# Kernel optimization log

Hardware: AMD Instinct MI355X
Metric: run time of the kernel (lower is better)

Reference implementation:

```python
import jax, jax.numpy as jnp
import numpy as np

D = 256
H = 8

def setup_inputs() -> dict:
    key = jax.random.key(0)
    ks = jax.random.split(key, 6)
    b, n = 4, 2048
    X = jax.random.normal(ks[0], (b, n, D), dtype=jnp.float32)
    s = 1.0 / np.sqrt(D)
    Wq = jax.random.normal(ks[1], (D, D * H), dtype=jnp.float32) * s
    Wk = jax.random.normal(ks[2], (D, D * H), dtype=jnp.float32) * s
    Wv = jax.random.normal(ks[3], (D, D * H), dtype=jnp.float32) * s
    Wo = jax.random.normal(ks[4], (D * H, D), dtype=jnp.float32) * (1.0 / np.sqrt(D * H))
    bo = jnp.zeros((D,), dtype=jnp.float32)
    return {"X": X, "Wq": Wq, "Wk": Wk, "Wv": Wv, "Wo": Wo, "bo": bo}

def reference(X, Wq, Wk, Wv, Wo, bo):
    b, n, _ = X.shape
    scale = D ** (-0.25)
    # project and split heads: [b, n, H, D]
    q = (X @ Wq).reshape(b, n, H, D) * scale
    k = (X @ Wk).reshape(b, n, H, D) * scale
    v = (X @ Wv).reshape(b, n, H, D)
    # attention scores [b, H, n, n]
    scores = jnp.einsum("bqhd,bkhd->bhqk", q, k)
    attn = jax.nn.softmax(scores, axis=-1)
    out = jnp.einsum("bhqk,bkhd->bqhd", attn, v).reshape(b, n, H * D)
    return out @ Wo + bo
```

## Files before the change

### kernel.cpp

```cpp
#include <hip/hip_runtime.h>
#include <hip/hip_bf16.h>
#include <stdint.h>


using short8 = __attribute__((ext_vector_type(8))) short;
using f32x4  = __attribute__((ext_vector_type(4))) float;
using f32x16 = __attribute__((ext_vector_type(16))) float;

#define MFMA16(a, b, c) __builtin_amdgcn_mfma_f32_16x16x32_bf16((a), (b), (c), 0, 0, 0)
#define MFMA32(a, b, c) __builtin_amdgcn_mfma_f32_32x32x16_bf16((a), (b), (c), 0, 0, 0)

#if __has_builtin(__builtin_amdgcn_exp2f)
#define EXP2(x) __builtin_amdgcn_exp2f(x)
#else
#define EXP2(x) exp2f(x)
#endif

__device__ __forceinline__ uint16_t f2bf(float f) {
  union { float f; uint32_t u; } v; v.f = f;
  uint32_t u = v.u;
  u += 0x7fffu + ((u >> 16) & 1u);
  return (uint16_t)(u >> 16);
}

__device__ __forceinline__ uint32_t cvtpk_bf16(float lo, float hi) {
  uint32_t r;
  asm("v_cvt_pk_bf16_f32 %0, %1, %2" : "=v"(r) : "v"(lo), "v"(hi));
  return r;
}

__device__ __forceinline__ void swap32(uint32_t& a, uint32_t& b) {
  asm volatile("v_permlane32_swap_b32 %0, %1" : "+v"(a), "+v"(b));
}

__device__ __forceinline__ void gll16(const void* g, void* l) {
  __builtin_amdgcn_global_load_lds(
      (const __attribute__((address_space(1))) void*)g,
      (__attribute__((address_space(3))) void*)l, 16, 0, 0);
}

__global__ __launch_bounds__(256) void cast_x_k(const float* __restrict__ X,
                                                uint16_t* __restrict__ Xb, int n4) {
  int i = blockIdx.x * 256 + threadIdx.x;
  if (i >= n4) return;
  float4 v = ((const float4*)X)[i];
  union { uint16_t u[4]; uint2 p; } r;
  r.u[0] = f2bf(v.x); r.u[1] = f2bf(v.y); r.u[2] = f2bf(v.z); r.u[3] = f2bf(v.w);
  ((uint2*)Xb)[i] = r.p;
}

__global__ __launch_bounds__(256) void tcast_k(const float* __restrict__ W,
                                               uint16_t* __restrict__ Wt,
                                               int R, int C, float scale) {
  __shared__ float T[64][65];
  int c0 = blockIdx.x * 64, r0 = blockIdx.y * 64;
  int tid = threadIdx.x;
  int cc = tid & 63;
  for (int rr = tid >> 6; rr < 64; rr += 4)
    T[rr][cc] = W[(size_t)(r0 + rr) * C + c0 + cc];
  __syncthreads();
  int n = tid >> 2, kb = (tid & 3) * 16;
  uint16_t* orow = Wt + (size_t)(c0 + n) * R + r0 + kb;
#pragma unroll
  for (int j = 0; j < 16; ++j) orow[j] = f2bf(T[kb + j][n] * scale);
}

template <int EPI>
__global__ __launch_bounds__(256) void gemm_bt_k(const uint16_t* __restrict__ A,
                                                 const uint16_t* __restrict__ Bt,
                                                 void* __restrict__ Cv,
                                                 const float* __restrict__ bias,
                                                 int M, int N, int K) {
  __shared__ uint16_t As[128 * 64];
  __shared__ uint16_t Bs[128 * 64];
  const int tid = threadIdx.x;
  const int wv = tid >> 6, lane = tid & 63;
  const int ql = lane & 15, gq = lane >> 4;
  const int wr = wv >> 1, wc = wv & 1;
  const int m0 = blockIdx.y * 128, n0 = blockIdx.x * 128;

  f32x4 acc[4][4];
#pragma unroll
  for (int i = 0; i < 4; ++i)
#pragma unroll
    for (int j = 0; j < 4; ++j) acc[i][j] = (f32x4){0.f, 0.f, 0.f, 0.f};

  const int nkb = K >> 6;
  for (int kb = 0; kb < nkb; ++kb) {
#pragma unroll
    for (int j = 0; j < 4; ++j) {
      int s = (wv * 4 + j) * 64 + lane;
      int row = s >> 3, c = s & 7;
      int gc = c ^ (row & 7);
      gll16(A + (size_t)(m0 + row) * K + kb * 64 + gc * 8, &As[(wv * 4 + j) * 512]);
      gll16(Bt + (size_t)(n0 + row) * K + kb * 64 + gc * 8, &Bs[(wv * 4 + j) * 512]);
    }
    __syncthreads();

    short8 af[4][2], bf[4][2];
#pragma unroll
    for (int mt = 0; mt < 4; ++mt)
#pragma unroll
      for (int kk = 0; kk < 2; ++kk) {
        int row = wr * 64 + mt * 16 + ql;
        int c = (kk * 4 + gq) ^ (row & 7);
        af[mt][kk] = *(const short8*)&As[row * 64 + c * 8];
      }
#pragma unroll
    for (int nt = 0; nt < 4; ++nt)
#pragma unroll
      for (int kk = 0; kk < 2; ++kk) {
        int row = wc * 64 + nt * 16 + ql;
        int c = (kk * 4 + gq) ^ (row & 7);
        bf[nt][kk] = *(const short8*)&Bs[row * 64 + c * 8];
      }
#pragma unroll
    for (int kk = 0; kk < 2; ++kk)
#pragma unroll
      for (int mt = 0; mt < 4; ++mt)
#pragma unroll
        for (int nt = 0; nt < 4; ++nt)
          acc[mt][nt] = MFMA16(af[mt][kk], bf[nt][kk], acc[mt][nt]);
    __syncthreads();
  }

#pragma unroll
  for (int mt = 0; mt < 4; ++mt)
#pragma unroll
    for (int nt = 0; nt < 4; ++nt)
#pragma unroll
      for (int r = 0; r < 4; ++r) {
        int m = m0 + wr * 64 + mt * 16 + gq * 4 + r;
        int n = n0 + wc * 64 + nt * 16 + ql;
        float v = acc[mt][nt][r];
        if (EPI == 0) {
          ((uint16_t*)Cv)[(size_t)m * N + n] = f2bf(v);
        } else {
          ((float*)Cv)[(size_t)m * N + n] = v + bias[n];
        }
      }
}

__global__ __launch_bounds__(512, 2) void attn2_k(const uint16_t* __restrict__ qk,
                                                  const uint16_t* __restrict__ vtws,
                                                  uint16_t* __restrict__ ctx,
                                                  int b0, int nb) {
  __shared__ uint16_t Ks[2][64 * 256];
  __shared__ uint16_t Vts[2][256 * 64];
  const int S = 2048;
  const int h = blockIdx.x & 7;
  const int t = blockIdx.x >> 3;
  const int bb = t >> 3, qb = t & 7;
  const int tid = threadIdx.x, w = tid >> 6, lane = tid & 63;
  const int l31 = lane & 31, hi = lane >> 5;
  const size_t SN = (size_t)nb * S;

  short8 qf[16];
  {
    const uint16_t* qrow =
        qk + (size_t)(bb * S + qb * 256 + w * 32 + l31) * 4096 + h * 256 + hi * 8;
#pragma unroll
    for (int ds = 0; ds < 16; ++ds) qf[ds] = *(const short8*)(qrow + ds * 16);
  }

  uint32_t ok[4], ov[4];
#pragma unroll
  for (int j = 0; j < 4; ++j) {
    int s = (j * 8 + w) * 64 + lane;
    int krow = s >> 5, kc = s & 31;
    int kgc = kc ^ (krow & 7);
    ok[j] = (uint32_t)(((bb * S + krow) * 4096 + 2048 + h * 256 + kgc * 8) * 2);
    int d = s >> 3, vc = s & 7;
    int vgc = vc ^ (d & 7);
    ov[j] = (uint32_t)((((h * 256 + d) * SN) + (size_t)bb * S + vgc * 8) * 2);
  }
  const uint32_t kstep = 64 * 4096 * 2;
  const uint32_t vstep = 64 * 2;

  const char* kgbase = (const char*)qk;
  const char* vgbase = (const char*)vtws;

  auto stage = [&](int buf, int kb) {
#pragma unroll
    for (int j = 0; j < 4; ++j) {
      gll16(kgbase + ok[j] + (uint32_t)kb * kstep, &Ks[buf][(j * 8 + w) * 512]);
      gll16(vgbase + ov[j] + (uint32_t)kb * vstep, &Vts[buf][(j * 8 + w) * 512]);
    }
  };

  f32x16 cacc[8];
#pragma unroll
  for (int db = 0; db < 8; ++db)
#pragma unroll
    for (int r = 0; r < 16; ++r) cacc[db][r] = 0.f;
  float m_run = -3e38f, l_run = 0.f;

  stage(0, 0);
  __syncthreads();

  const int rx = (l31 & 7) << 4;
  const int hi16 = hi << 4;

  auto sm_pv = [&](f32x16& s, int ksbase, const char* vbase) {
    float pm = fmaxf(
        fmaxf(fmaxf(fmaxf(s[0], s[1]), fmaxf(s[2], s[3])),
              fmaxf(fmaxf(s[4], s[5]), fmaxf(s[6], s[7]))),
        fmaxf(fmaxf(fmaxf(s[8], s[9]), fmaxf(s[10], s[11])),
              fmaxf(fmaxf(s[12], s[13]), fmaxf(s[14], s[15]))));
    pm = fmaxf(pm, __shfl_xor(pm, 32));

    if (__any(pm - m_run > 8.0f)) {
      float mn = fmaxf(m_run, pm);
      float al = EXP2(m_run - mn);
      m_run = mn;
      l_run *= al;
#pragma unroll
      for (int r = 0; r < 16; ++r) {
        float a = __shfl(al, (r & 3) + 8 * (r >> 2) + 4 * hi);
#pragma unroll
        for (int db = 0; db < 8; ++db) cacc[db][r] *= a;
      }
    }

    float ps = 0.f;
#pragma unroll
    for (int r = 0; r < 16; ++r) { s[r] = EXP2(s[r] - m_run); ps += s[r]; }
    ps += __shfl_xor(ps, 32);
    l_run += ps;

    uint32_t W[4][2];
#pragma unroll
    for (int g = 0; g < 4; ++g) {
      W[g][0] = cvtpk_bf16(s[4 * g], s[4 * g + 1]);
      W[g][1] = cvtpk_bf16(s[4 * g + 2], s[4 * g + 3]);
    }
    swap32(W[0][0], W[1][0]); swap32(W[0][1], W[1][1]);
    swap32(W[2][0], W[3][0]); swap32(W[2][1], W[3][1]);
    union U { uint32_t u[4]; short8 v; };
    U pa0, pa1;
    pa0.u[0] = W[0][0]; pa0.u[1] = W[0][1]; pa0.u[2] = W[1][0]; pa0.u[3] = W[1][1];
    pa1.u[0] = W[2][0]; pa1.u[1] = W[2][1]; pa1.u[2] = W[3][0]; pa1.u[3] = W[3][1];

    __builtin_amdgcn_s_setprio(1);
#pragma unroll
    for (int kh = 0; kh < 2; ++kh) {
      int voff = ((ksbase + kh) * 32 + hi16) ^ rx;
      short8 pv = kh ? pa1.v : pa0.v;
#pragma unroll
      for (int db = 0; db < 8; ++db) {
        short8 vf = *(const short8*)(vbase + (db * 32 + l31) * 128 + voff);
        cacc[db] = MFMA32(pv, vf, cacc[db]);
      }
    }
    __builtin_amdgcn_s_setprio(0);
  };

  for (int kb = 0; kb < 32; ++kb) {
    const int cur = kb & 1;
    if (kb < 31) stage(cur ^ 1, kb + 1);

    const char* kbase = (const char*)Ks[cur];
    const char* vbase = (const char*)Vts[cur];
    const char* kr0 = kbase + l31 * 512;
    const char* kr1 = kbase + (32 + l31) * 512;

    f32x16 sA, sB;
#pragma unroll
    for (int r = 0; r < 16; ++r) { sA[r] = 0.f; sB[r] = 0.f; }
    __builtin_amdgcn_s_setprio(1);
#pragma unroll
    for (int ds = 0; ds < 16; ++ds) {
      int off = (ds * 32 + hi16) ^ rx;
      short8 kA = *(const short8*)(kr0 + off);
      short8 kB = *(const short8*)(kr1 + off);
      sA = MFMA32(kA, qf[ds], sA);
      sB = MFMA32(kB, qf[ds], sB);
    }
    __builtin_amdgcn_s_setprio(0);

    sm_pv(sA, 0, vbase);
    sm_pv(sB, 2, vbase);

    __syncthreads();
  }

  float linv = 1.f / l_run;
  uint16_t* crow = ctx + (size_t)((b0 + bb) * S + qb * 256 + w * 32) * 2048 + h * 256;
#pragma unroll
  for (int r = 0; r < 16; ++r) {
    int qr = (r & 3) + 8 * (r >> 2) + 4 * hi;
    float lr = __shfl(linv, qr);
#pragma unroll
    for (int db = 0; db < 8; ++db)
      crow[(size_t)qr * 2048 + db * 32 + l31] = f2bf(cacc[db][r] * lr);
  }
}

extern "C" void kernel_launch(void* const* d_in, const int* in_sizes, int n_in,
                              void* d_out, int out_size, void* d_ws, size_t ws_size,
                              hipStream_t stream) {
  const float* X  = (const float*)d_in[0];
  const float* Wq = (const float*)d_in[1];
  const float* Wk = (const float*)d_in[2];
  const float* Wv = (const float*)d_in[3];
  const float* Wo = (const float*)d_in[4];
  const float* bo = (const float*)d_in[5];
  float* out = (float*)d_out;

  const int B = 4, S = 2048, Dm = 256, DH = 2048;
  (void)in_sizes; (void)n_in; (void)out_size; (void)ws_size;

  uint16_t* p = (uint16_t*)d_ws;
  uint16_t* Xb  = p; p += (size_t)B * S * Dm;
  uint16_t* Wqt = p; p += (size_t)DH * Dm;
  uint16_t* Wkt = p; p += (size_t)DH * Dm;
  uint16_t* Wvt = p; p += (size_t)DH * Dm;
  uint16_t* Wot = p; p += (size_t)Dm * DH;
  uint16_t* ctx = p; p += (size_t)B * S * DH;
  uint16_t* qkw = p; p += (size_t)B * S * (2 * DH);
  uint16_t* vtws = p;

  const float qs = 0.25f * 1.2011224087864498f;

  cast_x_k<<<dim3((B * S * Dm / 4 + 255) / 256), 256, 0, stream>>>(X, Xb, B * S * Dm / 4);
  tcast_k<<<dim3(DH / 64, Dm / 64), 256, 0, stream>>>(Wq, Wqt, Dm, DH, qs);
  tcast_k<<<dim3(DH / 64, Dm / 64), 256, 0, stream>>>(Wk, Wkt, Dm, DH, qs);
  tcast_k<<<dim3(DH / 64, Dm / 64), 256, 0, stream>>>(Wv, Wvt, Dm, DH, 1.0f);
  tcast_k<<<dim3(Dm / 64, DH / 64), 256, 0, stream>>>(Wo, Wot, DH, Dm, 1.0f);

  gemm_bt_k<0><<<dim3((2 * DH) / 128, (B * S) / 128), 256, 0, stream>>>(
      Xb, Wqt, qkw, nullptr, B * S, 2 * DH, Dm);
  gemm_bt_k<0><<<dim3((B * S) / 128, DH / 128), 256, 0, stream>>>(
      Wvt, Xb, vtws, nullptr, DH, B * S, Dm);
  attn2_k<<<dim3(64 * B), 512, 0, stream>>>(qkw, vtws, ctx, 0, B);
  gemm_bt_k<1><<<dim3(Dm / 128, (B * S) / 128), 256, 0, stream>>>(
      ctx, Wot, out, bo, B * S, Dm, DH);
}
```

Measured before the change: 274.7 us.

## Software-pipeline QK of next half-tile with softmax/PV of current

Splits each 64-key tile into two 32-key halves and rotates the score accumulators, so the QK MFMAs for the next half are issued before the softmax and PV of the current half. K is now prefetched two tiles ahead and V one tile ahead, on separate staging schedules. The aim is to overlap exp/max VALU work with matrix-core work and hide global-to-LDS latency better. The cost is an extra live f32x16 accumulator and more complex buffer-reuse timing, which adds register pressure and a risk of LDS hazards.

Result: slower. 307.1 us (+11.8%).

```diff
diff --git a/kernel.cpp b/kernel.cpp
--- a/kernel.cpp
+++ b/kernel.cpp
@@ -180,12 +180,15 @@
   const char* kgbase = (const char*)qk;
   const char* vgbase = (const char*)vtws;
 
-  auto stage = [&](int buf, int kb) {
-#pragma unroll
-    for (int j = 0; j < 4; ++j) {
-      gll16(kgbase + ok[j] + (uint32_t)kb * kstep, &Ks[buf][(j * 8 + w) * 512]);
-      gll16(vgbase + ov[j] + (uint32_t)kb * vstep, &Vts[buf][(j * 8 + w) * 512]);
-    }
+  auto stageK = [&](int u) {
+#pragma unroll
+    for (int j = 0; j < 4; ++j)
+      gll16(kgbase + ok[j] + (uint32_t)u * kstep, &Ks[u & 1][(j * 8 + w) * 512]);
+  };
+  auto stageV = [&](int u) {
+#pragma unroll
+    for (int j = 0; j < 4; ++j)
+      gll16(vgbase + ov[j] + (uint32_t)u * vstep, &Vts[u & 1][(j * 8 + w) * 512]);
   };
 
   f32x16 cacc[8];
@@ -195,13 +198,26 @@
     for (int r = 0; r < 16; ++r) cacc[db][r] = 0.f;
   float m_run = -3e38f, l_run = 0.f;
 
-  stage(0, 0);
-  __syncthreads();
-
   const int rx = (l31 & 7) << 4;
   const int hi16 = hi << 4;
 
-  auto sm_pv = [&](f32x16& s, int ksbase, const char* vbase) {
+  auto qk_half = [&](f32x16& s, int H) {
+    const char* kr =
+        (const char*)&Ks[(H >> 1) & 1][0] + ((H & 1) * 32 + l31) * 512;
+#pragma unroll
+    for (int r = 0; r < 16; ++r) s[r] = 0.f;
+    __builtin_amdgcn_s_setprio(1);
+#pragma unroll
+    for (int ds = 0; ds < 16; ++ds) {
+      int off = (ds * 32 + hi16) ^ rx;
+      s = MFMA32(*(const short8*)(kr + off), qf[ds], s);
+    }
+    __builtin_amdgcn_s_setprio(0);
+  };
+
+  auto sm_pv = [&](f32x16& s, int H) {
+    const char* vbase = (const char*)&Vts[(H >> 1) & 1][0];
+    const int ksbase = (H & 1) * 2;
     float pm = fmaxf(
         fmaxf(fmaxf(fmaxf(s[0], s[1]), fmaxf(s[2], s[3])),
               fmaxf(fmaxf(s[4], s[5]), fmaxf(s[6], s[7]))),
@@ -255,33 +271,26 @@
     __builtin_amdgcn_s_setprio(0);
   };
 
-  for (int kb = 0; kb < 32; ++kb) {
-    const int cur = kb & 1;
-    if (kb < 31) stage(cur ^ 1, kb + 1);
-
-    const char* kbase = (const char*)Ks[cur];
-    const char* vbase = (const char*)Vts[cur];
-    const char* kr0 = kbase + l31 * 512;
-    const char* kr1 = kbase + (32 + l31) * 512;
-
-    f32x16 sA, sB;
-#pragma unroll
-    for (int r = 0; r < 16; ++r) { sA[r] = 0.f; sB[r] = 0.f; }
-    __builtin_amdgcn_s_setprio(1);
-#pragma unroll
-    for (int ds = 0; ds < 16; ++ds) {
-      int off = (ds * 32 + hi16) ^ rx;
-      short8 kA = *(const short8*)(kr0 + off);
-      short8 kB = *(const short8*)(kr1 + off);
-      sA = MFMA32(kA, qf[ds], sA);
-      sB = MFMA32(kB, qf[ds], sB);
-    }
-    __builtin_amdgcn_s_setprio(0);
-
-    sm_pv(sA, 0, vbase);
-    sm_pv(sB, 2, vbase);
-
-    __syncthreads();
+  auto body = [&](int H, f32x16& cur, f32x16& nxt) {
+    if (H & 1) {
+      int tt = H >> 1;
+      if (tt <= 29) stageK(tt + 2);
+      if (tt >= 1 && tt <= 30) stageV(tt + 1);
+    }
+    if (H < 63) qk_half(nxt, H + 1);
+    sm_pv(cur, H);
+    if ((H & 1) && H < 63) __syncthreads();
+  };
+
+  stageK(0); stageK(1); stageV(0); stageV(1);
+  __syncthreads();
+
+  f32x16 sEven, sOdd;
+  qk_half(sEven, 0);
+
+  for (int tt = 0; tt < 32; ++tt) {
+    body(2 * tt, sEven, sOdd);
+    body(2 * tt + 1, sOdd, sEven);
   }
 
   float linv = 1.f / l_run;
```

## Software-pipeline attention so QK of next tile interleaves with PV of previous

Applied to the files above, without the earlier changes.

Splits K and V staging and restructures the main loop so that the QK^T MFMAs for key tile t are interleaved with the PV MFMAs for tile t-1. There is a prologue QK-only step and an epilogue PV-only step. Softmax for both 32-row halves is merged into one pass with a single shared running-max update per 64-key tile. The intent is to hide softmax latency and keep the matrix units busy across stages. The cost is extra live registers for the four packed P fragments, which could raise register pressure.

New measurement: 270.7 us. Within noise of the previous version (-1.4%).

```diff
diff --git a/kernel.cpp b/kernel.cpp
--- a/kernel.cpp
+++ b/kernel.cpp
@@ -167,9 +167,9 @@
 #pragma unroll
   for (int j = 0; j < 4; ++j) {
     int s = (j * 8 + w) * 64 + lane;
-    int krow = s >> 5, kc = s & 31;
-    int kgc = kc ^ (krow & 7);
-    ok[j] = (uint32_t)(((bb * S + krow) * 4096 + 2048 + h * 256 + kgc * 8) * 2);
+    int krw = s >> 5, kc = s & 31;
+    int kgc = kc ^ (krw & 7);
+    ok[j] = (uint32_t)(((bb * S + krw) * 4096 + 2048 + h * 256 + kgc * 8) * 2);
     int d = s >> 3, vc = s & 7;
     int vgc = vc ^ (d & 7);
     ov[j] = (uint32_t)((((h * 256 + d) * SN) + (size_t)bb * S + vgc * 8) * 2);
@@ -180,12 +180,15 @@
   const char* kgbase = (const char*)qk;
   const char* vgbase = (const char*)vtws;
 
-  auto stage = [&](int buf, int kb) {
-#pragma unroll
-    for (int j = 0; j < 4; ++j) {
+  auto stageK = [&](int buf, int kb) {
+#pragma unroll
+    for (int j = 0; j < 4; ++j)
       gll16(kgbase + ok[j] + (uint32_t)kb * kstep, &Ks[buf][(j * 8 + w) * 512]);
+  };
+  auto stageV = [&](int buf, int kb) {
+#pragma unroll
+    for (int j = 0; j < 4; ++j)
       gll16(vgbase + ov[j] + (uint32_t)kb * vstep, &Vts[buf][(j * 8 + w) * 512]);
-    }
   };
 
   f32x16 cacc[8];
@@ -194,19 +197,81 @@
 #pragma unroll
     for (int r = 0; r < 16; ++r) cacc[db][r] = 0.f;
   float m_run = -3e38f, l_run = 0.f;
-
-  stage(0, 0);
-  __syncthreads();
+  short8 pa0, pa1, pa2, pa3;
 
   const int rx = (l31 & 7) << 4;
   const int hi16 = hi << 4;
 
-  auto sm_pv = [&](f32x16& s, int ksbase, const char* vbase) {
+  f32x16 sA, sB;
+
+  auto qk_only = [&](int cur) {
+    const char* kr0 = (const char*)Ks[cur] + l31 * 512;
+    const char* kr1 = kr0 + 32 * 512;
+#pragma unroll
+    for (int r = 0; r < 16; ++r) { sA[r] = 0.f; sB[r] = 0.f; }
+    __builtin_amdgcn_s_setprio(1);
+#pragma unroll
+    for (int i = 0; i < 16; ++i) {
+      int off = (i * 32 + hi16) ^ rx;
+      sA = MFMA32(*(const short8*)(kr0 + off), qf[i], sA);
+      sB = MFMA32(*(const short8*)(kr1 + off), qf[i], sB);
+    }
+    __builtin_amdgcn_s_setprio(0);
+  };
+
+  auto qk_pv = [&](int cur) {
+    const char* kr0 = (const char*)Ks[cur] + l31 * 512;
+    const char* kr1 = kr0 + 32 * 512;
+    const char* vb = (const char*)Vts[cur ^ 1];
+#pragma unroll
+    for (int r = 0; r < 16; ++r) { sA[r] = 0.f; sB[r] = 0.f; }
+    __builtin_amdgcn_s_setprio(1);
+#pragma unroll
+    for (int i = 0; i < 16; ++i) {
+      int off = (i * 32 + hi16) ^ rx;
+      sA = MFMA32(*(const short8*)(kr0 + off), qf[i], sA);
+      sB = MFMA32(*(const short8*)(kr1 + off), qf[i], sB);
+#pragma unroll
+      for (int u = 0; u < 2; ++u) {
+        const int idx = 2 * i + u;
+        const int ks = idx >> 3, db = idx & 7;
+        int voff = (ks * 32 + hi16) ^ rx;
+        short8 vf = *(const short8*)(vb + (db * 32 + l31) * 128 + voff);
+        short8 p = (ks == 0) ? pa0 : (ks == 1) ? pa1 : (ks == 2) ? pa2 : pa3;
+        cacc[db] = MFMA32(p, vf, cacc[db]);
+      }
+    }
+    __builtin_amdgcn_s_setprio(0);
+  };
+
+  auto pv_only = [&](int slot) {
+    const char* vb = (const char*)Vts[slot];
+    __builtin_amdgcn_s_setprio(1);
+#pragma unroll
+    for (int ks = 0; ks < 4; ++ks) {
+      int voff = (ks * 32 + hi16) ^ rx;
+      short8 p = (ks == 0) ? pa0 : (ks == 1) ? pa1 : (ks == 2) ? pa2 : pa3;
+#pragma unroll
+      for (int db = 0; db < 8; ++db) {
+        short8 vf = *(const short8*)(vb + (db * 32 + l31) * 128 + voff);
+        cacc[db] = MFMA32(p, vf, cacc[db]);
+      }
+    }
+    __builtin_amdgcn_s_setprio(0);
+  };
+
+  auto sm_pack = [&]() {
     float pm = fmaxf(
-        fmaxf(fmaxf(fmaxf(s[0], s[1]), fmaxf(s[2], s[3])),
-              fmaxf(fmaxf(s[4], s[5]), fmaxf(s[6], s[7]))),
-        fmaxf(fmaxf(fmaxf(s[8], s[9]), fmaxf(s[10], s[11])),
-              fmaxf(fmaxf(s[12], s[13]), fmaxf(s[14], s[15]))));
+        fmaxf(fmaxf(fmaxf(sA[0], sA[1]), fmaxf(sA[2], sA[3])),
+              fmaxf(fmaxf(sA[4], sA[5]), fmaxf(sA[6], sA[7]))),
+        fmaxf(fmaxf(fmaxf(sA[8], sA[9]), fmaxf(sA[10], sA[11])),
+              fmaxf(fmaxf(sA[12], sA[13]), fmaxf(sA[14], sA[15]))));
+    float pmB = fmaxf(
+        fmaxf(fmaxf(fmaxf(sB[0], sB[1]), fmaxf(sB[2], sB[3])),
+              fmaxf(fmaxf(sB[4], sB[5]), fmaxf(sB[6], sB[7]))),
+        fmaxf(fmaxf(fmaxf(sB[8], sB[9]), fmaxf(sB[10], sB[11])),
+              fmaxf(fmaxf(sB[12], sB[13]), fmaxf(sB[14], sB[15]))));
+    pm = fmaxf(pm, pmB);
     pm = fmaxf(pm, __shfl_xor(pm, 32));
 
     if (__any(pm - m_run > 8.0f)) {
@@ -224,65 +289,51 @@
 
     float ps = 0.f;
 #pragma unroll
-    for (int r = 0; r < 16; ++r) { s[r] = EXP2(s[r] - m_run); ps += s[r]; }
+    for (int r = 0; r < 16; ++r) { sA[r] = EXP2(sA[r] - m_run); ps += sA[r]; }
+#pragma unroll
+    for (int r = 0; r < 16; ++r) { sB[r] = EXP2(sB[r] - m_run); ps += sB[r]; }
     ps += __shfl_xor(ps, 32);
     l_run += ps;
 
-    uint32_t W[4][2];
+    uint32_t WA[4][2], WB[4][2];
 #pragma unroll
     for (int g = 0; g < 4; ++g) {
-      W[g][0] = cvtpk_bf16(s[4 * g], s[4 * g + 1]);
-      W[g][1] = cvtpk_bf16(s[4 * g + 2], s[4 * g + 3]);
-    }
-    swap32(W[0][0], W[1][0]); swap32(W[0][1], W[1][1]);
-    swap32(W[2][0], W[3][0]); swap32(W[2][1], W[3][1]);
+      WA[g][0] = cvtpk_bf16(sA[4 * g], sA[4 * g + 1]);
+      WA[g][1] = cvtpk_bf16(sA[4 * g + 2], sA[4 * g + 3]);
+      WB[g][0] = cvtpk_bf16(sB[4 * g], sB[4 * g + 1]);
+      WB[g][1] = cvtpk_bf16(sB[4 * g + 2], sB[4 * g + 3]);
+    }
+    swap32(WA[0][0], WA[1][0]); swap32(WA[0][1], WA[1][1]);
+    swap32(WA[2][0], WA[3][0]); swap32(WA[2][1], WA[3][1]);
+    swap32(WB[0][0], WB[1][0]); swap32(WB[0][1], WB[1][1]);
+    swap32(WB[2][0], WB[3][0]); swap32(WB[2][1], WB[3][1]);
     union U { uint32_t u[4]; short8 v; };
-    U pa0, pa1;
-    pa0.u[0] = W[0][0]; pa0.u[1] = W[0][1]; pa0.u[2] = W[1][0]; pa0.u[3] = W[1][1];
-    pa1.u[0] = W[2][0]; pa1.u[1] = W[2][1]; pa1.u[2] = W[3][0]; pa1.u[3] = W[3][1];
-
-    __builtin_amdgcn_s_setprio(1);
-#pragma unroll
-    for (int kh = 0; kh < 2; ++kh) {
-      int voff = ((ksbase + kh) * 32 + hi16) ^ rx;
-      short8 pv = kh ? pa1.v : pa0.v;
-#pragma unroll
-      for (int db = 0; db < 8; ++db) {
-        short8 vf = *(const short8*)(vbase + (db * 32 + l31) * 128 + voff);
-        cacc[db] = MFMA32(pv, vf, cacc[db]);
-      }
-    }
-    __builtin_amdgcn_s_setprio(0);
-  };
-
-  for (int kb = 0; kb < 32; ++kb) {
-    const int cur = kb & 1;
-    if (kb < 31) stage(cur ^ 1, kb + 1);
-
-    const char* kbase = (const char*)Ks[cur];
-    const char* vbase = (const char*)Vts[cur];
-    const char* kr0 = kbase + l31 * 512;
-    const char* kr1 = kbase + (32 + l31) * 512;
-
-    f32x16 sA, sB;
-#pragma unroll
-    for (int r = 0; r < 16; ++r) { sA[r] = 0.f; sB[r] = 0.f; }
-    __builtin_amdgcn_s_setprio(1);
-#pragma unroll
-    for (int ds = 0; ds < 16; ++ds) {
-      int off = (ds * 32 + hi16) ^ rx;
-      short8 kA = *(const short8*)(kr0 + off);
-      short8 kB = *(const short8*)(kr1 + off);
-      sA = MFMA32(kA, qf[ds], sA);
-      sB = MFMA32(kB, qf[ds], sB);
-    }
-    __builtin_amdgcn_s_setprio(0);
-
-    sm_pv(sA, 0, vbase);
-    sm_pv(sB, 2, vbase);
-
+    U a0, a1, b0, b1;
+    a0.u[0] = WA[0][0]; a0.u[1] = WA[0][1]; a0.u[2] = WA[1][0]; a0.u[3] = WA[1][1];
+    a1.u[0] = WA[2][0]; a1.u[1] = WA[2][1]; a1.u[2] = WA[3][0]; a1.u[3] = WA[3][1];
+    b0.u[0] = WB[0][0]; b0.u[1] = WB[0][1]; b0.u[2] = WB[1][0]; b0.u[3] = WB[1][1];
+    b1.u[0] = WB[2][0]; b1.u[1] = WB[2][1]; b1.u[2] = WB[3][0]; b1.u[3] = WB[3][1];
+    pa0 = a0.v; pa1 = a1.v; pa2 = b0.v; pa3 = b1.v;
+  };
+
+  stageK(0, 0);
+  __syncthreads();
+
+  stageK(1, 1);
+  stageV(0, 0);
+  qk_only(0);
+  sm_pack();
+  __syncthreads();
+
+  for (int tt = 1; tt < 32; ++tt) {
+    const int cur = tt & 1;
+    if (tt < 31) stageK(cur ^ 1, tt + 1);
+    stageV(cur, tt);
+    qk_pv(cur);
+    sm_pack();
     __syncthreads();
   }
+  pv_only(1);
 
   float linv = 1.f / l_run;
   uint16_t* crow = ctx + (size_t)((b0 + bb) * S + qb * 256 + w * 32) * 2048 + h * 256;
```
